# Optimization experiments

Hardware: AMD Instinct MI355X
Metric: run time of the kernel (lower is better)

## Reference

```python
import jax, jax.numpy as jnp
import numpy as np

B, T, Dx, H, K = 32, 4096, 128, 128, 10


def setup_inputs() -> dict:
    key = jax.random.key(0)
    ks = jax.random.split(key, 11)
    s = 1.0 / np.sqrt(H)  # PyTorch GRU init range

    def p(k, shape):
        return jax.random.uniform(k, shape, jnp.float32, -s, s)

    return {
        "x": jax.random.normal(ks[0], (B, T, Dx), jnp.float32),
        # forward-direction GRU params (gate order: r, z, n as in PyTorch)
        "W_ih_f": p(ks[1], (3 * H, Dx)),
        "W_hh_f": p(ks[2], (3 * H, H)),
        "b_ih_f": p(ks[3], (3 * H,)),
        "b_hh_f": p(ks[4], (3 * H,)),
        # backward-direction GRU params
        "W_ih_b": p(ks[5], (3 * H, Dx)),
        "W_hh_b": p(ks[6], (3 * H, H)),
        "b_ih_b": p(ks[7], (3 * H,)),
        "b_hh_b": p(ks[8], (3 * H,)),
        # final linear classifier
        "W_fc": p(ks[9], (K, 2 * H)),
        "b_fc": p(ks[10], (K,)),
    }


def _gru_scan(x, Wih, Whh, bih, bhh, reverse):
    """Single-direction GRU over time. x: [B,T,Dx] -> [B,T,H]."""
    # Precompute all input projections at once: [T, B, 3H]
    xp = jnp.einsum('btd,gd->tbg', x, Wih) + bih
    Whh_T = Whh.T
    Hd = Whh.shape[1]

    def cell(h, xt):
        hp = h @ Whh_T + bhh            # [B, 3H]
        xr, xz, xn = jnp.split(xt, 3, axis=-1)
        hr, hz, hn = jnp.split(hp, 3, axis=-1)
        r = jax.nn.sigmoid(xr + hr)
        z = jax.nn.sigmoid(xz + hz)
        n = jnp.tanh(xn + r * hn)
        h_new = (1.0 - z) * n + z * h
        return h_new, h_new

    h0 = jnp.zeros((x.shape[0], Hd), x.dtype)
    _, hs = jax.lax.scan(cell, h0, xp, reverse=reverse)  # [T, B, H]
    return jnp.transpose(hs, (1, 0, 2))


def reference(x, W_ih_f, W_hh_f, b_ih_f, b_hh_f,
              W_ih_b, W_hh_b, b_ih_b, b_hh_b, W_fc, b_fc):
    hf = _gru_scan(x, W_ih_f, W_hh_f, b_ih_f, b_hh_f, reverse=False)
    hb = _gru_scan(x, W_ih_b, W_hh_b, b_ih_b, b_hh_b, reverse=True)
    h = jnp.concatenate([hf, hb], axis=-1)  # [B, T, 2H]
    return h @ W_fc.T + b_fc                # [B, T, K]
```

## Files before the change

### kernel.cpp

```cpp
#include <hip/hip_runtime.h>
#include <cstdint>
#include <cstddef>

#define T_LEN   4096
#define B_SZ    32
#define H_DIM   128
#define DX      128
#define K_CLS   10
#define CHUNK   32
#define NCHUNKS (T_LEN / CHUNK)
#define XA_LD   136
#define XP_LD   520
#define HI_LD   136

typedef _Float16 half2v  __attribute__((ext_vector_type(2)));
typedef _Float16 half4   __attribute__((ext_vector_type(4)));
typedef _Float16 half8   __attribute__((ext_vector_type(8)));
typedef float    floatx4 __attribute__((ext_vector_type(4)));

#define LGKM_BARRIER() do {                                   \
    asm volatile("s_waitcnt lgkmcnt(0)" ::: "memory");        \
    __builtin_amdgcn_s_barrier();                             \
    asm volatile("" ::: "memory");                            \
  } while (0)

__global__ void __launch_bounds__(256) init_out_kernel(float* __restrict__ out,
                                                       const float* __restrict__ bfc) {
  int i = blockIdx.x * 256 + threadIdx.x;
  if (i < B_SZ * T_LEN * K_CLS) out[i] = bfc[i % K_CLS];
}

__global__ void __launch_bounds__(256, 1)
gru_bidir_kernel(const float* __restrict__ x,
                 const float* __restrict__ Wih_f, const float* __restrict__ Whh_f,
                 const float* __restrict__ bih_f, const float* __restrict__ bhh_f,
                 const float* __restrict__ Wih_b, const float* __restrict__ Whh_b,
                 const float* __restrict__ bih_b, const float* __restrict__ bhh_b,
                 const float* __restrict__ Wfc, float* __restrict__ out) {
  const int tid = threadIdx.x;
  const int bid = blockIdx.x;
  const int b   = bid & (B_SZ - 1);
  const int dir = bid >> 5;

  const float* Wih = dir ? Wih_b : Wih_f;
  const float* Whh = dir ? Whh_b : Whh_f;
  const float* bih = dir ? bih_b : bih_f;
  const float* bhh = dir ? bhh_b : bhh_f;

  const int lane = tid & 63;
  const int wv   = tid >> 6;
  const int col  = lane & 15;
  const int quad = lane >> 4;
  const int j0   = wv * 32 + col;
  const int j1   = j0 + 16;

  __shared__ __align__(16) _Float16 xA[CHUNK][XA_LD];
  __shared__ __align__(16) _Float16 xPL[CHUNK][XP_LD];
  __shared__ __align__(16) _Float16 hist[CHUNK + 1][HI_LD];

  const float LOG2E = 1.44269504f;

  half8 whf[2][3][4];
  half8 wif[2][3][4];
#pragma unroll
  for (int ct = 0; ct < 2; ++ct) {
    const int jct = wv * 32 + ct * 16 + col;
#pragma unroll
    for (int g = 0; g < 3; ++g) {
      const float gs = (g == 2) ? 2.0f * LOG2E : LOG2E;
#pragma unroll
      for (int kt = 0; kt < 4; ++kt) {
        const float* sh = Whh + (size_t)(g * H_DIM + jct) * H_DIM + kt * 32 + quad * 8;
        const float* si = Wih + (size_t)(g * H_DIM + jct) * DX + kt * 32 + quad * 8;
        half8 vh, vi;
#pragma unroll
        for (int e = 0; e < 8; ++e) {
          vh[e] = (_Float16)(sh[e] * gs);
          vi[e] = (_Float16)(si[e] * gs);
        }
        whf[ct][g][kt] = vh;
        wif[ct][g][kt] = vi;
      }
    }
  }
  float br[2], bz[2], bn[2];
  floatx4 cNbv[2];
#pragma unroll
  for (int ct = 0; ct < 2; ++ct) {
    const int jct = wv * 32 + ct * 16 + col;
    br[ct] = (bih[jct] + bhh[jct]) * LOG2E;
    bz[ct] = (bih[H_DIM + jct] + bhh[H_DIM + jct]) * LOG2E;
    bn[ct] = bih[2 * H_DIM + jct] * (2.0f * LOG2E);
    float bh = bhh[2 * H_DIM + jct] * (2.0f * LOG2E);
    cNbv[ct] = (floatx4){bh, bh, bh, bh};
  }

  half8 fcf[4];
  if (wv < 2) {
#pragma unroll
    for (int kt = 0; kt < 4; ++kt) {
      half8 v;
#pragma unroll
      for (int e = 0; e < 8; ++e) {
        int k = kt * 32 + quad * 8 + e;
        v[e] = (col < K_CLS) ? (_Float16)Wfc[(size_t)col * (2 * H_DIM) + dir * H_DIM + k]
                             : (_Float16)0.f;
      }
      fcf[kt] = v;
    }
  }

  if (tid < H_DIM) hist[0][tid] = (_Float16)0.f;

  const int s_row = tid >> 3;
  const int cb    = (tid & 7) * 16;
  float4 px0, px1, px2, px3;
  {
    int t0 = dir ? (T_LEN - 1 - s_row) : s_row;
    const float* xr = x + ((size_t)b * T_LEN + t0) * DX + cb;
    px0 = *(const float4*)xr;        px1 = *(const float4*)(xr + 4);
    px2 = *(const float4*)(xr + 8);  px3 = *(const float4*)(xr + 12);
  }

  float hold0 = 0.f, hold1 = 0.f;
  const floatx4 z4 = {0.f, 0.f, 0.f, 0.f};
  __syncthreads();

  for (int c = 0; c < NCHUNKS; ++c) {
    {
      half8 lo, hi;
      lo[0] = (_Float16)px0.x; lo[1] = (_Float16)px0.y; lo[2] = (_Float16)px0.z; lo[3] = (_Float16)px0.w;
      lo[4] = (_Float16)px1.x; lo[5] = (_Float16)px1.y; lo[6] = (_Float16)px1.z; lo[7] = (_Float16)px1.w;
      hi[0] = (_Float16)px2.x; hi[1] = (_Float16)px2.y; hi[2] = (_Float16)px2.z; hi[3] = (_Float16)px2.w;
      hi[4] = (_Float16)px3.x; hi[5] = (_Float16)px3.y; hi[6] = (_Float16)px3.z; hi[7] = (_Float16)px3.w;
      *(half8*)&xA[s_row][cb] = lo;
      *(half8*)&xA[s_row][cb + 8] = hi;
    }
    LGKM_BARRIER();

#pragma unroll
    for (int mt = 0; mt < 2; ++mt) {
      half8 af[4];
#pragma unroll
      for (int kt = 0; kt < 4; ++kt)
        af[kt] = *(const half8*)&xA[mt * 16 + col][kt * 32 + quad * 8];
#pragma unroll
      for (int ct = 0; ct < 2; ++ct) {
        floatx4 pr = z4, pz = z4, pn = z4;
#pragma unroll
        for (int kt = 0; kt < 4; ++kt) {
          pr = __builtin_amdgcn_mfma_f32_16x16x32_f16(af[kt], wif[ct][0][kt], pr, 0, 0, 0);
          pz = __builtin_amdgcn_mfma_f32_16x16x32_f16(af[kt], wif[ct][1][kt], pz, 0, 0, 0);
          pn = __builtin_amdgcn_mfma_f32_16x16x32_f16(af[kt], wif[ct][2][kt], pn, 0, 0, 0);
        }
        const int jw = (ct ? j1 : j0) * 4;
#pragma unroll
        for (int i = 0; i < 4; ++i) {
          half4 w;
          w[0] = (_Float16)(pr[i] + br[ct]);
          w[1] = (_Float16)(pz[i] + bz[ct]);
          w[2] = (_Float16)(pn[i] + bn[ct]);
          w[3] = (_Float16)0.f;
          *(half4*)&xPL[mt * 16 + quad * 4 + i][jw] = w;
        }
      }
    }

    if (c + 1 < NCHUNKS) {
      int s  = (c + 1) * CHUNK + s_row;
      int t0 = dir ? (T_LEN - 1 - s) : s;
      const float* xr = x + ((size_t)b * T_LEN + t0) * DX + cb;
      px0 = *(const float4*)xr;        px1 = *(const float4*)(xr + 4);
      px2 = *(const float4*)(xr + 8);  px3 = *(const float4*)(xr + 12);
    }
    LGKM_BARRIER();

    uint2 xv0 = *(const uint2*)&xPL[0][j0 * 4];
    uint2 xv1 = *(const uint2*)&xPL[0][j1 * 4];

#pragma unroll
    for (int s = 0; s < CHUNK; ++s) {
      half8 haf[4];
#pragma unroll
      for (int kt = 0; kt < 4; ++kt)
        haf[kt] = *(const half8*)&hist[s][kt * 32 + quad * 8];
      uint2 xvn0 = *(const uint2*)&xPL[(s + 1) & (CHUNK - 1)][j0 * 4];
      uint2 xvn1 = *(const uint2*)&xPL[(s + 1) & (CHUNK - 1)][j1 * 4];

      half2v xa0 = __builtin_bit_cast(half2v, xv0.x);
      half2v xb0 = __builtin_bit_cast(half2v, xv0.y);
      half2v xa1 = __builtin_bit_cast(half2v, xv1.x);
      half2v xb1 = __builtin_bit_cast(half2v, xv1.y);
      float xr0 = (float)xa0.x, xz0 = (float)xa0.y, xn0 = (float)xb0.x;
      float xr1 = (float)xa1.x, xz1 = (float)xa1.y, xn1 = (float)xb1.x;
      floatx4 cR0 = {xr0, xr0, xr0, xr0}, cZ0 = {xz0, xz0, xz0, xz0};
      floatx4 cR1 = {xr1, xr1, xr1, xr1}, cZ1 = {xz1, xz1, xz1, xz1};

      floatx4 a0[3][4], a1[3][4];
#pragma unroll
      for (int g = 0; g < 3; ++g) {
#pragma unroll
        for (int kt = 0; kt < 4; ++kt) {
          floatx4 c0 = (kt == 0) ? ((g == 0) ? cR0 : (g == 1) ? cZ0 : cNbv[0]) : z4;
          a0[g][kt] = __builtin_amdgcn_mfma_f32_16x16x32_f16(haf[kt], whf[0][g][kt], c0, 0, 0, 0);
        }
      }
#pragma unroll
      for (int g = 0; g < 3; ++g) {
#pragma unroll
        for (int kt = 0; kt < 4; ++kt) {
          floatx4 c1 = (kt == 0) ? ((g == 0) ? cR1 : (g == 1) ? cZ1 : cNbv[1]) : z4;
          a1[g][kt] = __builtin_amdgcn_mfma_f32_16x16x32_f16(haf[kt], whf[1][g][kt], c1, 0, 0, 0);
        }
      }

      {
        float ar = (a0[0][0][0] + a0[0][1][0]) + (a0[0][2][0] + a0[0][3][0]);
        float rr = __builtin_amdgcn_rcpf(1.f + __builtin_amdgcn_exp2f(-ar));
        float az = (a0[1][0][0] + a0[1][1][0]) + (a0[1][2][0] + a0[1][3][0]);
        float zz = __builtin_amdgcn_rcpf(1.f + __builtin_amdgcn_exp2f(-az));
        float an = (a0[2][0][0] + a0[2][1][0]) + (a0[2][2][0] + a0[2][3][0]);
        float yn = fmaf(rr, an, xn0);
        float t  = __builtin_amdgcn_exp2f(-fmaxf(yn, -80.f));
        float nn = fmaf(2.f, __builtin_amdgcn_rcpf(1.f + t), -1.f);
        hold0 = fmaf(zz, hold0 - nn, nn);
      }
      {
        float ar = (a1[0][0][0] + a1[0][1][0]) + (a1[0][2][0] + a1[0][3][0]);
        float rr = __builtin_amdgcn_rcpf(1.f + __builtin_amdgcn_exp2f(-ar));
        float az = (a1[1][0][0] + a1[1][1][0]) + (a1[1][2][0] + a1[1][3][0]);
        float zz = __builtin_amdgcn_rcpf(1.f + __builtin_amdgcn_exp2f(-az));
        float an = (a1[2][0][0] + a1[2][1][0]) + (a1[2][2][0] + a1[2][3][0]);
        float yn = fmaf(rr, an, xn1);
        float t  = __builtin_amdgcn_exp2f(-fmaxf(yn, -80.f));
        float nn = fmaf(2.f, __builtin_amdgcn_rcpf(1.f + t), -1.f);
        hold1 = fmaf(zz, hold1 - nn, nn);
      }

      if (quad == 0) {
        hist[s + 1][j0] = (_Float16)hold0;
        hist[s + 1][j1] = (_Float16)hold1;
      }
      LGKM_BARRIER();
      xv0 = xvn0;
      xv1 = xvn1;
    }

    if (wv < 2) {
      floatx4 fa = z4;
#pragma unroll
      for (int kt = 0; kt < 4; ++kt) {
        half8 af = *(const half8*)&hist[1 + wv * 16 + col][kt * 32 + quad * 8];
        fa = __builtin_amdgcn_mfma_f32_16x16x32_f16(af, fcf[kt], fa, 0, 0, 0);
      }
      if (col < K_CLS) {
#pragma unroll
        for (int i = 0; i < 4; ++i) {
          int t  = c * CHUNK + wv * 16 + quad * 4 + i;
          int tt = dir ? (T_LEN - 1 - t) : t;
          atomicAdd(out + ((size_t)b * T_LEN + tt) * K_CLS + col, fa[i]);
        }
      }
    } else if (wv == 2) {
      ((unsigned int*)&hist[0][0])[lane] = ((const unsigned int*)&hist[CHUNK][0])[lane];
    }
  }
}

extern "C" void kernel_launch(void* const* d_in, const int* in_sizes, int n_in,
                              void* d_out, int out_size, void* d_ws, size_t ws_size,
                              hipStream_t stream) {
  (void)in_sizes; (void)n_in; (void)d_ws; (void)ws_size; (void)out_size;
  const float* x     = (const float*)d_in[0];
  const float* Wih_f = (const float*)d_in[1];
  const float* Whh_f = (const float*)d_in[2];
  const float* bih_f = (const float*)d_in[3];
  const float* bhh_f = (const float*)d_in[4];
  const float* Wih_b = (const float*)d_in[5];
  const float* Whh_b = (const float*)d_in[6];
  const float* bih_b = (const float*)d_in[7];
  const float* bhh_b = (const float*)d_in[8];
  const float* Wfc   = (const float*)d_in[9];
  const float* bfc   = (const float*)d_in[10];
  float* out = (float*)d_out;

  const int n_out = B_SZ * T_LEN * K_CLS;
  init_out_kernel<<<(n_out + 255) / 256, 256, 0, stream>>>(out, bfc);
  gru_bidir_kernel<<<B_SZ * 2, 256, 0, stream>>>(x, Wih_f, Whh_f, bih_f, bhh_f,
                                                 Wih_b, Whh_b, bih_b, bhh_b, Wfc, out);
}
```

Baseline: 2.001 ms.

## Fuse forward and backward directions into one 512-thread block per batch

Each block now holds both directions for one batch element: threads 0-255 run the forward GRU and threads 256-511 the backward one, with shared buffers duplicated per group. The grid shrinks from 64 to 32 blocks. The change also removes the clamp on the tanh exponent argument. A risk is that the two groups now share every block-wide barrier, so each step waits on both recurrences in lockstep. Dropping the clamp may also produce inf for very negative inputs, although rcp(1+inf) still yields 0.

```diff
diff --git a/kernel.cpp b/kernel.cpp
--- a/kernel.cpp
+++ b/kernel.cpp
@@ -30,17 +30,18 @@
   if (i < B_SZ * T_LEN * K_CLS) out[i] = bfc[i % K_CLS];
 }
 
-__global__ void __launch_bounds__(256, 1)
+__global__ void __launch_bounds__(512, 2)
 gru_bidir_kernel(const float* __restrict__ x,
                  const float* __restrict__ Wih_f, const float* __restrict__ Whh_f,
                  const float* __restrict__ bih_f, const float* __restrict__ bhh_f,
                  const float* __restrict__ Wih_b, const float* __restrict__ Whh_b,
                  const float* __restrict__ bih_b, const float* __restrict__ bhh_b,
                  const float* __restrict__ Wfc, float* __restrict__ out) {
-  const int tid = threadIdx.x;
-  const int bid = blockIdx.x;
-  const int b   = bid & (B_SZ - 1);
-  const int dir = bid >> 5;
+  const int tid  = threadIdx.x;
+  const int b    = blockIdx.x;
+  const int grp  = tid >> 8;
+  const int ltid = tid & 255;
+  const int dir  = grp;
 
   const float* Wih = dir ? Wih_b : Wih_f;
   const float* Whh = dir ? Whh_b : Whh_f;
@@ -48,15 +49,15 @@
   const float* bhh = dir ? bhh_b : bhh_f;
 
   const int lane = tid & 63;
-  const int wv   = tid >> 6;
+  const int lwv  = (tid >> 6) & 3;
   const int col  = lane & 15;
   const int quad = lane >> 4;
-  const int j0   = wv * 32 + col;
+  const int j0   = lwv * 32 + col;
   const int j1   = j0 + 16;
 
-  __shared__ __align__(16) _Float16 xA[CHUNK][XA_LD];
-  __shared__ __align__(16) _Float16 xPL[CHUNK][XP_LD];
-  __shared__ __align__(16) _Float16 hist[CHUNK + 1][HI_LD];
+  __shared__ __align__(16) _Float16 xA[2][CHUNK][XA_LD];
+  __shared__ __align__(16) _Float16 xPL[2][CHUNK][XP_LD];
+  __shared__ __align__(16) _Float16 hist[2][CHUNK + 1][HI_LD];
 
   const float LOG2E = 1.44269504f;
 
@@ -64,7 +65,7 @@
   half8 wif[2][3][4];
 #pragma unroll
   for (int ct = 0; ct < 2; ++ct) {
-    const int jct = wv * 32 + ct * 16 + col;
+    const int jct = lwv * 32 + ct * 16 + col;
 #pragma unroll
     for (int g = 0; g < 3; ++g) {
       const float gs = (g == 2) ? 2.0f * LOG2E : LOG2E;
@@ -87,7 +88,7 @@
   floatx4 cNbv[2];
 #pragma unroll
   for (int ct = 0; ct < 2; ++ct) {
-    const int jct = wv * 32 + ct * 16 + col;
+    const int jct = lwv * 32 + ct * 16 + col;
     br[ct] = (bih[jct] + bhh[jct]) * LOG2E;
     bz[ct] = (bih[H_DIM + jct] + bhh[H_DIM + jct]) * LOG2E;
     bn[ct] = bih[2 * H_DIM + jct] * (2.0f * LOG2E);
@@ -96,7 +97,7 @@
   }
 
   half8 fcf[4];
-  if (wv < 2) {
+  if (lwv < 2) {
 #pragma unroll
     for (int kt = 0; kt < 4; ++kt) {
       half8 v;
@@ -110,10 +111,10 @@
     }
   }
 
-  if (tid < H_DIM) hist[0][tid] = (_Float16)0.f;
-
-  const int s_row = tid >> 3;
-  const int cb    = (tid & 7) * 16;
+  if (ltid < H_DIM) hist[grp][0][ltid] = (_Float16)0.f;
+
+  const int s_row = ltid >> 3;
+  const int cb    = (ltid & 7) * 16;
   float4 px0, px1, px2, px3;
   {
     int t0 = dir ? (T_LEN - 1 - s_row) : s_row;
@@ -133,8 +134,8 @@
       lo[4] = (_Float16)px1.x; lo[5] = (_Float16)px1.y; lo[6] = (_Float16)px1.z; lo[7] = (_Float16)px1.w;
       hi[0] = (_Float16)px2.x; hi[1] = (_Float16)px2.y; hi[2] = (_Float16)px2.z; hi[3] = (_Float16)px2.w;
       hi[4] = (_Float16)px3.x; hi[5] = (_Float16)px3.y; hi[6] = (_Float16)px3.z; hi[7] = (_Float16)px3.w;
-      *(half8*)&xA[s_row][cb] = lo;
-      *(half8*)&xA[s_row][cb + 8] = hi;
+      *(half8*)&xA[grp][s_row][cb] = lo;
+      *(half8*)&xA[grp][s_row][cb + 8] = hi;
     }
     LGKM_BARRIER();
 
@@ -143,7 +144,7 @@
       half8 af[4];
 #pragma unroll
       for (int kt = 0; kt < 4; ++kt)
-        af[kt] = *(const half8*)&xA[mt * 16 + col][kt * 32 + quad * 8];
+        af[kt] = *(const half8*)&xA[grp][mt * 16 + col][kt * 32 + quad * 8];
 #pragma unroll
       for (int ct = 0; ct < 2; ++ct) {
         floatx4 pr = z4, pz = z4, pn = z4;
@@ -161,7 +162,7 @@
           w[1] = (_Float16)(pz[i] + bz[ct]);
           w[2] = (_Float16)(pn[i] + bn[ct]);
           w[3] = (_Float16)0.f;
-          *(half4*)&xPL[mt * 16 + quad * 4 + i][jw] = w;
+          *(half4*)&xPL[grp][mt * 16 + quad * 4 + i][jw] = w;
         }
       }
     }
@@ -175,17 +176,17 @@
     }
     LGKM_BARRIER();
 
-    uint2 xv0 = *(const uint2*)&xPL[0][j0 * 4];
-    uint2 xv1 = *(const uint2*)&xPL[0][j1 * 4];
+    uint2 xv0 = *(const uint2*)&xPL[grp][0][j0 * 4];
+    uint2 xv1 = *(const uint2*)&xPL[grp][0][j1 * 4];
 
 #pragma unroll
     for (int s = 0; s < CHUNK; ++s) {
       half8 haf[4];
 #pragma unroll
       for (int kt = 0; kt < 4; ++kt)
-        haf[kt] = *(const half8*)&hist[s][kt * 32 + quad * 8];
-      uint2 xvn0 = *(const uint2*)&xPL[(s + 1) & (CHUNK - 1)][j0 * 4];
-      uint2 xvn1 = *(const uint2*)&xPL[(s + 1) & (CHUNK - 1)][j1 * 4];
+        haf[kt] = *(const half8*)&hist[grp][s][kt * 32 + quad * 8];
+      uint2 xvn0 = *(const uint2*)&xPL[grp][(s + 1) & (CHUNK - 1)][j0 * 4];
+      uint2 xvn1 = *(const uint2*)&xPL[grp][(s + 1) & (CHUNK - 1)][j1 * 4];
 
       half2v xa0 = __builtin_bit_cast(half2v, xv0.x);
       half2v xb0 = __builtin_bit_cast(half2v, xv0.y);
@@ -221,7 +222,7 @@
         float zz = __builtin_amdgcn_rcpf(1.f + __builtin_amdgcn_exp2f(-az));
         float an = (a0[2][0][0] + a0[2][1][0]) + (a0[2][2][0] + a0[2][3][0]);
         float yn = fmaf(rr, an, xn0);
-        float t  = __builtin_amdgcn_exp2f(-fmaxf(yn, -80.f));
+        float t  = __builtin_amdgcn_exp2f(-yn);
         float nn = fmaf(2.f, __builtin_amdgcn_rcpf(1.f + t), -1.f);
         hold0 = fmaf(zz, hold0 - nn, nn);
       }
@@ -232,37 +233,37 @@
         float zz = __builtin_amdgcn_rcpf(1.f + __builtin_amdgcn_exp2f(-az));
         float an = (a1[2][0][0] + a1[2][1][0]) + (a1[2][2][0] + a1[2][3][0]);
         float yn = fmaf(rr, an, xn1);
-        float t  = __builtin_amdgcn_exp2f(-fmaxf(yn, -80.f));
+        float t  = __builtin_amdgcn_exp2f(-yn);
         float nn = fmaf(2.f, __builtin_amdgcn_rcpf(1.f + t), -1.f);
         hold1 = fmaf(zz, hold1 - nn, nn);
       }
 
       if (quad == 0) {
-        hist[s + 1][j0] = (_Float16)hold0;
-        hist[s + 1][j1] = (_Float16)hold1;
+        hist[grp][s + 1][j0] = (_Float16)hold0;
+        hist[grp][s + 1][j1] = (_Float16)hold1;
       }
       LGKM_BARRIER();
       xv0 = xvn0;
       xv1 = xvn1;
     }
 
-    if (wv < 2) {
+    if (lwv < 2) {
       floatx4 fa = z4;
 #pragma unroll
       for (int kt = 0; kt < 4; ++kt) {
-        half8 af = *(const half8*)&hist[1 + wv * 16 + col][kt * 32 + quad * 8];
+        half8 af = *(const half8*)&hist[grp][1 + lwv * 16 + col][kt * 32 + quad * 8];
         fa = __builtin_amdgcn_mfma_f32_16x16x32_f16(af, fcf[kt], fa, 0, 0, 0);
       }
       if (col < K_CLS) {
 #pragma unroll
         for (int i = 0; i < 4; ++i) {
-          int t  = c * CHUNK + wv * 16 + quad * 4 + i;
+          int t  = c * CHUNK + lwv * 16 + quad * 4 + i;
           int tt = dir ? (T_LEN - 1 - t) : t;
           atomicAdd(out + ((size_t)b * T_LEN + tt) * K_CLS + col, fa[i]);
         }
       }
-    } else if (wv == 2) {
-      ((unsigned int*)&hist[0][0])[lane] = ((const unsigned int*)&hist[CHUNK][0])[lane];
+    } else if (lwv == 2) {
+      ((unsigned int*)&hist[grp][0][0])[lane] = ((const unsigned int*)&hist[grp][CHUNK][0])[lane];
     }
   }
 }
@@ -286,6 +287,6 @@
 
   const int n_out = B_SZ * T_LEN * K_CLS;
   init_out_kernel<<<(n_out + 255) / 256, 256, 0, stream>>>(out, bfc);
-  gru_bidir_kernel<<<B_SZ * 2, 256, 0, stream>>>(x, Wih_f, Whh_f, bih_f, bhh_f,
-                                                 Wih_b, Whh_b, bih_b, bhh_b, Wfc, out);
+  gru_bidir_kernel<<<B_SZ, 512, 0, stream>>>(x, Wih_f, Whh_f, bih_f, bhh_f,
+                                             Wih_b, Whh_b, bih_b, bhh_b, Wfc, out);
 }
```

New measurement: 3.748 ms. +87.3%, slower.
